# Performance work log

Measured on AMD Instinct MI355X. Metric: run time of the kernel, lower is better.

The kernel has to match this reference:

```python
import math
import jax, jax.numpy as jnp
from jax import lax
import numpy as np

L, B, S, D, H, F = 12, 8, 512, 768, 12, 3072
DH = D // H
REL_POS_BINS, MAX_REL_POS = 32, 128
REL_2D_POS_BINS, MAX_REL_2D_POS = 64, 256
LN_EPS = 1e-12


def _rel_bucket(rel, num_buckets, max_distance):
    # bidirectional relative_position_bucket as in LayoutLMv2
    num_buckets = num_buckets // 2
    ret = (rel > 0).astype(jnp.int32) * num_buckets
    n = jnp.abs(rel)
    max_exact = num_buckets // 2
    is_small = n < max_exact
    n_safe = jnp.maximum(n, 1)  # avoid log(0); masked by is_small anyway
    val_if_large = max_exact + (
        jnp.log(n_safe.astype(jnp.float32) / max_exact)
        / math.log(max_distance / max_exact) * (num_buckets - max_exact)
    ).astype(jnp.int32)
    val_if_large = jnp.minimum(val_if_large, num_buckets - 1)
    return ret + jnp.where(is_small, n.astype(jnp.int32), val_if_large)


def _layernorm(x, g, b):
    mu = jnp.mean(x, axis=-1, keepdims=True)
    var = jnp.var(x, axis=-1, keepdims=True)
    return (x - mu) * lax.rsqrt(var + LN_EPS) * g + b


def _encoder(hidden_states, attention_mask, position_ids, bbox,
             qkv_w, q_bias, v_bias, attn_out_w, attn_out_b, ln1_g, ln1_b,
             inter_w, inter_b, ffn_out_w, ffn_out_b, ln2_g, ln2_b,
             rel_pos_table, rel_x_table, rel_y_table):
    b, s, d = hidden_states.shape
    h = rel_pos_table.shape[1]
    dh = d // h
    # 1D relative position bias: [B,H,S,S]
    rel = position_ids[:, None, :] - position_ids[:, :, None]  # [B,S,S], rel[b,i,j]=p[j]-p[i]
    rp = _rel_bucket(rel, REL_POS_BINS, MAX_REL_POS)
    bias = jnp.transpose(rel_pos_table[rp], (0, 3, 1, 2))
    # 2D spatial bias from bbox x (coord 0) and y (coord 3)
    cx = bbox[:, :, 0]
    cy = bbox[:, :, 3]
    bx = _rel_bucket(cx[:, None, :] - cx[:, :, None], REL_2D_POS_BINS, MAX_REL_2D_POS)
    by = _rel_bucket(cy[:, None, :] - cy[:, :, None], REL_2D_POS_BINS, MAX_REL_2D_POS)
    bias = bias + jnp.transpose(rel_x_table[bx] + rel_y_table[by], (0, 3, 1, 2))
    mask = attention_mask.astype(bool)  # [B,1,1,S], True = masked
    inv_sqrt_dh = 1.0 / math.sqrt(dh)

    def layer(carry, p):
        (qw, qb, vb, aow, aob, g1, b1, iw, ib, fow, fob, g2, b2) = p
        qkv = carry @ qw                      # [B,S,3D] (fast_qkv, no bias)
        q, k, v = jnp.split(qkv, 3, axis=-1)
        q = (q + qb) * inv_sqrt_dh
        v = v + vb
        q = q.reshape(b, s, h, dh)
        k = k.reshape(b, s, h, dh)
        v = v.reshape(b, s, h, dh)
        scores = jnp.einsum('bihd,bjhd->bhij', q, k) + bias
        scores = jnp.where(mask, -jnp.inf, scores.astype(jnp.float32))
        probs = jax.nn.softmax(scores, axis=-1).astype(carry.dtype)
        ctx = jnp.einsum('bhij,bjhd->bihd', probs, v).reshape(b, s, d)
        attn = _layernorm(ctx @ aow + aob + carry, g1, b1)
        ff = jax.nn.gelu(attn @ iw + ib, approximate=False)
        out = _layernorm(ff @ fow + fob + attn, g2, b2)
        return out, None

    params = (qkv_w, q_bias, v_bias, attn_out_w, attn_out_b, ln1_g, ln1_b,
              inter_w, inter_b, ffn_out_w, ffn_out_b, ln2_g, ln2_b)
    out, _ = lax.scan(layer, hidden_states, params)
    return out


def setup_inputs() -> dict:
    key = jax.random.key(0)
    ks = jax.random.split(key, 12)
    w = 0.02
    inp = {
        'hidden_states': jax.random.normal(ks[0], (B, S, D), jnp.float32),
        'attention_mask': jax.random.randint(ks[1], (B, 1, 1, S), 0, 2).astype(jnp.int32),
        'position_ids': jnp.broadcast_to(jnp.arange(S, dtype=jnp.int64), (B, S)),
        'bbox': jax.random.randint(ks[2], (B, S, 4), 0, 1000).astype(jnp.int64),
        'qkv_w': jax.random.normal(ks[3], (L, D, 3 * D), jnp.float32) * w,
        'q_bias': jnp.zeros((L, D), jnp.float32),
        'v_bias': jnp.zeros((L, D), jnp.float32),
        'attn_out_w': jax.random.normal(ks[4], (L, D, D), jnp.float32) * w,
        'attn_out_b': jnp.zeros((L, D), jnp.float32),
        'ln1_g': jnp.ones((L, D), jnp.float32),
        'ln1_b': jnp.zeros((L, D), jnp.float32),
        'inter_w': jax.random.normal(ks[5], (L, D, F), jnp.float32) * w,
        'inter_b': jnp.zeros((L, F), jnp.float32),
        'ffn_out_w': jax.random.normal(ks[6], (L, F, D), jnp.float32) * w,
        'ffn_out_b': jnp.zeros((L, D), jnp.float32),
        'ln2_g': jnp.ones((L, D), jnp.float32),
        'ln2_b': jnp.zeros((L, D), jnp.float32),
        'rel_pos_table': jax.random.normal(ks[7], (REL_POS_BINS, H), jnp.float32) * w,
        'rel_x_table': jax.random.normal(ks[8], (REL_2D_POS_BINS, H), jnp.float32) * w,
        'rel_y_table': jax.random.normal(ks[9], (REL_2D_POS_BINS, H), jnp.float32) * w,
    }
    return inp


def reference(hidden_states, attention_mask, position_ids, bbox,
              qkv_w, q_bias, v_bias, attn_out_w, attn_out_b, ln1_g, ln1_b,
              inter_w, inter_b, ffn_out_w, ffn_out_b, ln2_g, ln2_b,
              rel_pos_table, rel_x_table, rel_y_table):
    return _encoder(hidden_states, attention_mask, position_ids, bbox,
                    qkv_w, q_bias, v_bias, attn_out_w, attn_out_b, ln1_g, ln1_b,
                    inter_w, inter_b, ffn_out_w, ffn_out_b, ln2_g, ln2_b,
                    rel_pos_table, rel_x_table, rel_y_table)
```

## Files before the change

kernel.cpp:

```cpp
#include <hip/hip_runtime.h>
#include <hip/hip_bf16.h>
#include <cstdint>

#define LCONST 12
#define BCONST 8
#define SCONST 512
#define DCONST 768
#define HCONST 12
#define FCONST 3072
#define DH 64

typedef __bf16 bf16x8 __attribute__((ext_vector_type(8)));
typedef float f32x4 __attribute__((ext_vector_type(4)));

__device__ __forceinline__ int rbucket(int rel, int nb2, int maxex) {
    int ret = (rel > 0) ? nb2 : 0;
    int n = (rel < 0) ? -rel : rel;
    if (n < maxex) return ret + n;
    const float inv_ln16 = 0.36067376022224085f;
    int v = maxex + (int)(logf((float)n / (float)maxex) * inv_ln16 * (float)(nb2 - maxex));
    if (v > nb2 - 1) v = nb2 - 1;
    return ret + v;
}

__global__ __launch_bounds__(256) void build_idx_kernel(
        const int* __restrict__ pos, const int* __restrict__ bbox,
        int* __restrict__ idx) {
    size_t t = (size_t)blockIdx.x * 256 + threadIdx.x;
    int j = (int)(t & 511);
    int i = (int)((t >> 9) & 511);
    int b = (int)(t >> 18);
    int rp = rbucket(pos[b * SCONST + j] - pos[b * SCONST + i], 16, 8);
    int cxi = bbox[((size_t)b * SCONST + i) * 4 + 0];
    int cxj = bbox[((size_t)b * SCONST + j) * 4 + 0];
    int cyi = bbox[((size_t)b * SCONST + i) * 4 + 3];
    int cyj = bbox[((size_t)b * SCONST + j) * 4 + 3];
    int bx = rbucket(cxj - cxi, 32, 16);
    int by = rbucket(cyj - cyi, 32, 16);
    idx[t] = rp | (bx << 5) | (by << 11);
}

__global__ __launch_bounds__(256) void cvt_kernel(const float* __restrict__ in,
                                                  __bf16* __restrict__ out, int n) {
    int t = blockIdx.x * 256 + threadIdx.x;
    if (t < n) out[t] = (__bf16)in[t];
}

__global__ __launch_bounds__(256) void transpose_cvt_kernel(
        const float* __restrict__ in, __bf16* __restrict__ out, int R, int C) {
    __shared__ float tile[32][33];
    int nct = C >> 5;
    int c0 = (blockIdx.x % nct) << 5;
    int r0 = (blockIdx.x / nct) << 5;
    int tx = threadIdx.x & 31, ty = threadIdx.x >> 5;
#pragma unroll
    for (int i = 0; i < 32; i += 8)
        tile[ty + i][tx] = in[(size_t)(r0 + ty + i) * C + c0 + tx];
    __syncthreads();
#pragma unroll
    for (int i = 0; i < 32; i += 8)
        out[(size_t)(c0 + ty + i) * R + r0 + tx] = (__bf16)tile[tx][ty + i];
}

template <int MODE>
__global__ __launch_bounds__(256) void gemm_kernel(
        const __bf16* __restrict__ A, const __bf16* __restrict__ Bt,
        int M, int N, int K,
        const float* __restrict__ cbias, const float* __restrict__ vbias,
        const float* __restrict__ resid, float* __restrict__ outF,
        __bf16* __restrict__ outQ, __bf16* __restrict__ outK,
        __bf16* __restrict__ outV, __bf16* __restrict__ outB) {
    __shared__ __align__(16) __bf16 As[128 * 32];
    __shared__ __align__(16) __bf16 Bs[128 * 32];
    int tid = threadIdx.x;
    int wid = tid >> 6, lane = tid & 63, quad = lane >> 4, l16 = lane & 15;
    int nTM = M >> 7;
    int tileM = (blockIdx.x % nTM) << 7;
    int tileN = (blockIdx.x / nTM) << 7;
    int wm = wid >> 1, wn = wid & 1;

    int srow = lane >> 2;
    int scol = (lane & 3) << 3;
    const __bf16* Ag = A + (size_t)(tileM + wid * 32 + srow) * K + scol;
    const __bf16* Bg = Bt + (size_t)(tileN + wid * 32 + srow) * K + scol;
    __bf16* Asl = As + (wid * 32 + srow) * 32 + scol;
    __bf16* Bsl = Bs + (wid * 32 + srow) * 32 + scol;

    f32x4 acc[4][4] = {};

    for (int k0 = 0; k0 < K; k0 += 32) {
        uint4 a0 = *(const uint4*)(Ag + k0);
        uint4 a1 = *(const uint4*)(Ag + (size_t)16 * K + k0);
        uint4 b0 = *(const uint4*)(Bg + k0);
        uint4 b1 = *(const uint4*)(Bg + (size_t)16 * K + k0);
        *(uint4*)Asl = a0;
        *(uint4*)(Asl + 16 * 32) = a1;
        *(uint4*)Bsl = b0;
        *(uint4*)(Bsl + 16 * 32) = b1;
        __syncthreads();
        bf16x8 af[4], bfr[4];
#pragma unroll
        for (int mt = 0; mt < 4; mt++)
            af[mt] = *(const bf16x8*)&As[(wm * 64 + mt * 16 + l16) * 32 + quad * 8];
#pragma unroll
        for (int nt = 0; nt < 4; nt++)
            bfr[nt] = *(const bf16x8*)&Bs[(wn * 64 + nt * 16 + l16) * 32 + quad * 8];
#pragma unroll
        for (int mt = 0; mt < 4; mt++)
#pragma unroll
            for (int nt = 0; nt < 4; nt++)
                acc[mt][nt] = __builtin_amdgcn_mfma_f32_16x16x32_bf16(
                        af[mt], bfr[nt], acc[mt][nt], 0, 0, 0);
        __syncthreads();
    }

#pragma unroll
    for (int mt = 0; mt < 4; mt++)
#pragma unroll
        for (int nt = 0; nt < 4; nt++)
#pragma unroll
            for (int r = 0; r < 4; r++) {
                int row = tileM + wm * 64 + mt * 16 + quad * 4 + r;
                int col = tileN + wn * 64 + nt * 16 + l16;
                float v = acc[mt][nt][r];
                if (MODE == 0) {
                    int b = row >> 9, s = row & 511;
                    if (col < 768) {
                        int h = col >> 6, dh = col & 63;
                        float q = (v + cbias[col]) * 0.125f;
                        outQ[(((size_t)b * HCONST + h) * SCONST + s) * DH + dh] = (__bf16)q;
                    } else if (col < 1536) {
                        int c2 = col - 768;
                        int h = c2 >> 6, dh = c2 & 63;
                        outK[(((size_t)b * HCONST + h) * SCONST + s) * DH + dh] = (__bf16)v;
                    } else {
                        int c2 = col - 1536;
                        int h = c2 >> 6, dh = c2 & 63;
                        float vv = v + vbias[c2];
                        outV[(((size_t)b * HCONST + h) * DH + dh) * SCONST + s] = (__bf16)vv;
                    }
                } else if (MODE == 1 || MODE == 3) {
                    size_t o = (size_t)row * N + col;
                    outF[o] = v + cbias[col] + resid[o];
                } else {
                    float u = v + cbias[col];
                    float g = 0.5f * u * (1.0f + erff(u * 0.70710678118654752f));
                    outB[(size_t)row * N + col] = (__bf16)g;
                }
            }
}

__global__ __launch_bounds__(256) void attn_kernel(
        const __bf16* __restrict__ qbuf, const __bf16* __restrict__ kbuf,
        const __bf16* __restrict__ vbuf, const int* __restrict__ idx,
        const int* __restrict__ amask, const float* __restrict__ tpg,
        const float* __restrict__ txg, const float* __restrict__ tyg,
        __bf16* __restrict__ ctx) {
    int bh = blockIdx.x >> 3;
    int i0 = (blockIdx.x & 7) << 6;
    int b = bh / HCONST, h = bh % HCONST;

    __shared__ __align__(16) __bf16 Ks[64 * 64];
    __shared__ __align__(16) __bf16 Vs[64 * 64];
    __shared__ __align__(16) __bf16 Ps[4][16 * 64];
    __shared__ float tp[32], tx[64], ty[64];
    __shared__ float mk[512];

    int tid = threadIdx.x;
    if (tid < 32) tp[tid] = tpg[tid * HCONST + h];
    if (tid < 64) {
        tx[tid] = txg[tid * HCONST + h];
        ty[tid] = tyg[tid * HCONST + h];
    }
    for (int j = tid; j < 512; j += 256)
        mk[j] = amask[b * SCONST + j] ? -INFINITY : 0.0f;
    __syncthreads();

    int wid = tid >> 6, lane = tid & 63, quad = lane >> 4, l16 = lane & 15;

    const __bf16* qrow = qbuf + ((size_t)bh * SCONST + i0 + wid * 16 + l16) * DH;
    bf16x8 qf0 = *(const bf16x8*)(qrow + quad * 8);
    bf16x8 qf1 = *(const bf16x8*)(qrow + 32 + quad * 8);

    const __bf16* kg = kbuf + (size_t)bh * SCONST * DH;
    const __bf16* vg = vbuf + (size_t)bh * DH * SCONST;

    f32x4 O[4] = {};
    float m_r[4] = {-1e30f, -1e30f, -1e30f, -1e30f};
    float l_r[4] = {0.f, 0.f, 0.f, 0.f};

    for (int j0 = 0; j0 < SCONST; j0 += 64) {
        const uint4* ksrc = (const uint4*)(kg + (size_t)j0 * DH);
        ((uint4*)Ks)[tid] = ksrc[tid];
        ((uint4*)Ks)[tid + 256] = ksrc[tid + 256];
        for (int c = tid; c < 512; c += 256) {
            int dh = c >> 3, cc = c & 7;
            ((uint4*)Vs)[c] = *(const uint4*)(vg + (size_t)dh * SCONST + j0 + cc * 8);
        }
        __syncthreads();

        float sc[4][4];
#pragma unroll
        for (int jt = 0; jt < 4; jt++) {
            f32x4 a = {};
            bf16x8 kf0 = *(const bf16x8*)&Ks[(jt * 16 + l16) * 64 + quad * 8];
            bf16x8 kf1 = *(const bf16x8*)&Ks[(jt * 16 + l16) * 64 + 32 + quad * 8];
            a = __builtin_amdgcn_mfma_f32_16x16x32_bf16(qf0, kf0, a, 0, 0, 0);
            a = __builtin_amdgcn_mfma_f32_16x16x32_bf16(qf1, kf1, a, 0, 0, 0);
#pragma unroll
            for (int r = 0; r < 4; r++) {
                int i = i0 + wid * 16 + quad * 4 + r;
                int j = j0 + jt * 16 + l16;
                int pk = idx[((size_t)b * SCONST + i) * SCONST + j];
                float bias = tp[pk & 31] + tx[(pk >> 5) & 63] + ty[(pk >> 11) & 63];
                sc[jt][r] = a[r] + bias + mk[j];
            }
        }

        float p[4][4];
#pragma unroll
        for (int r = 0; r < 4; r++) {
            float mb = fmaxf(fmaxf(sc[0][r], sc[1][r]), fmaxf(sc[2][r], sc[3][r]));
#pragma unroll
            for (int m = 1; m < 16; m <<= 1) mb = fmaxf(mb, __shfl_xor(mb, m, 64));
            float mn = fmaxf(m_r[r], mb);
            float alpha = __expf(m_r[r] - mn);
            m_r[r] = mn;
            float ls = 0.f;
#pragma unroll
            for (int jt = 0; jt < 4; jt++) {
                float pv = __expf(sc[jt][r] - mn);
                p[jt][r] = pv;
                ls += pv;
            }
#pragma unroll
            for (int m = 1; m < 16; m <<= 1) ls += __shfl_xor(ls, m, 64);
            l_r[r] = l_r[r] * alpha + ls;
#pragma unroll
            for (int nt = 0; nt < 4; nt++) O[nt][r] *= alpha;
        }

        __bf16* pl = &Ps[wid][0];
#pragma unroll
        for (int jt = 0; jt < 4; jt++)
#pragma unroll
            for (int r = 0; r < 4; r++)
                pl[(quad * 4 + r) * 64 + jt * 16 + l16] = (__bf16)p[jt][r];

        bf16x8 pa0 = *(const bf16x8*)&pl[l16 * 64 + quad * 8];
        bf16x8 pa1 = *(const bf16x8*)&pl[l16 * 64 + 32 + quad * 8];
#pragma unroll
        for (int nt = 0; nt < 4; nt++) {
            bf16x8 vb0 = *(const bf16x8*)&Vs[(nt * 16 + l16) * 64 + quad * 8];
            bf16x8 vb1 = *(const bf16x8*)&Vs[(nt * 16 + l16) * 64 + 32 + quad * 8];
            O[nt] = __builtin_amdgcn_mfma_f32_16x16x32_bf16(pa0, vb0, O[nt], 0, 0, 0);
            O[nt] = __builtin_amdgcn_mfma_f32_16x16x32_bf16(pa1, vb1, O[nt], 0, 0, 0);
        }
        __syncthreads();
    }

#pragma unroll
    for (int nt = 0; nt < 4; nt++)
#pragma unroll
        for (int r = 0; r < 4; r++) {
            int i = i0 + wid * 16 + quad * 4 + r;
            int dh = nt * 16 + l16;
            float o = O[nt][r] / l_r[r];
            ctx[((size_t)b * SCONST + i) * DCONST + h * DH + dh] = (__bf16)o;
        }
}

__global__ __launch_bounds__(256) void ln_kernel(
        const float* __restrict__ in, const float* __restrict__ g,
        const float* __restrict__ bb, float* __restrict__ outF,
        __bf16* __restrict__ outB) {
    __shared__ float red[4];
    int row = blockIdx.x, t = threadIdx.x;
    const float* x = in + (size_t)row * DCONST;
    float v0 = x[t], v1 = x[t + 256], v2 = x[t + 512];
    float s = v0 + v1 + v2;
#pragma unroll
    for (int m = 1; m < 64; m <<= 1) s += __shfl_xor(s, m, 64);
    if ((t & 63) == 0) red[t >> 6] = s;
    __syncthreads();
    s = red[0] + red[1] + red[2] + red[3];
    __syncthreads();
    float mu = s * (1.0f / 768.0f);
    float d0 = v0 - mu, d1 = v1 - mu, d2 = v2 - mu;
    float q = d0 * d0 + d1 * d1 + d2 * d2;
#pragma unroll
    for (int m = 1; m < 64; m <<= 1) q += __shfl_xor(q, m, 64);
    if ((t & 63) == 0) red[t >> 6] = q;
    __syncthreads();
    q = red[0] + red[1] + red[2] + red[3];
    float rstd = rsqrtf(q * (1.0f / 768.0f) + 1e-12f);
    float y0 = d0 * rstd * g[t] + bb[t];
    float y1 = d1 * rstd * g[t + 256] + bb[t + 256];
    float y2 = d2 * rstd * g[t + 512] + bb[t + 512];
    size_t o = (size_t)row * DCONST;
    outF[o + t] = y0;
    outF[o + t + 256] = y1;
    outF[o + t + 512] = y2;
    outB[o + t] = (__bf16)y0;
    outB[o + t + 256] = (__bf16)y1;
    outB[o + t + 512] = (__bf16)y2;
}

extern "C" void kernel_launch(void* const* d_in, const int* in_sizes, int n_in,
                              void* d_out, int out_size, void* d_ws, size_t ws_size,
                              hipStream_t stream) {
    const float* hidden = (const float*)d_in[0];
    const int* amask = (const int*)d_in[1];
    const int* pos = (const int*)d_in[2];
    const int* bbox = (const int*)d_in[3];
    const float* qkv_w = (const float*)d_in[4];
    const float* q_bias = (const float*)d_in[5];
    const float* v_bias = (const float*)d_in[6];
    const float* aow = (const float*)d_in[7];
    const float* aob = (const float*)d_in[8];
    const float* ln1g = (const float*)d_in[9];
    const float* ln1b = (const float*)d_in[10];
    const float* iw = (const float*)d_in[11];
    const float* ib = (const float*)d_in[12];
    const float* fow = (const float*)d_in[13];
    const float* fob = (const float*)d_in[14];
    const float* ln2g = (const float*)d_in[15];
    const float* ln2b = (const float*)d_in[16];
    const float* tpt = (const float*)d_in[17];
    const float* txt = (const float*)d_in[18];
    const float* tyt = (const float*)d_in[19];
    float* out = (float*)d_out;

    char* w = (char*)d_ws;
    auto carve = [&](size_t bytes) {
        char* p = w;
        w += (bytes + 255) & ~(size_t)255;
        return p;
    };
    const size_t MT = 4096;
    __bf16* wqT = (__bf16*)carve((size_t)2304 * 768 * 2);
    __bf16* waT = (__bf16*)carve((size_t)768 * 768 * 2);
    __bf16* wiT = (__bf16*)carve((size_t)3072 * 768 * 2);
    __bf16* wfT = (__bf16*)carve((size_t)768 * 3072 * 2);
    __bf16* qbuf = (__bf16*)carve(MT * 768 * 2);
    __bf16* kbuf = (__bf16*)carve(MT * 768 * 2);
    __bf16* vbuf = (__bf16*)carve(MT * 768 * 2);
    __bf16* xbf = (__bf16*)carve(MT * 768 * 2);
    __bf16* ctxbf = (__bf16*)carve(MT * 768 * 2);
    float* attnf = (float*)carve(MT * 768 * 4);
    __bf16* attnbf = (__bf16*)carve(MT * 768 * 2);
    __bf16* ffbf = (__bf16*)carve(MT * 3072 * 2);
    float* t1 = (float*)carve(MT * 768 * 4);
    int* idxb = (int*)carve((size_t)BCONST * SCONST * SCONST * 4);

    build_idx_kernel<<<(BCONST * SCONST * SCONST) / 256, 256, 0, stream>>>(pos, bbox, idxb);
    cvt_kernel<<<(int)(MT * 768 / 256), 256, 0, stream>>>(hidden, xbf, (int)(MT * 768));

    for (int l = 0; l < LCONST; l++) {
        transpose_cvt_kernel<<<(2304 / 32) * (768 / 32), 256, 0, stream>>>(
                qkv_w + (size_t)l * 768 * 2304, wqT, 768, 2304);
        transpose_cvt_kernel<<<(768 / 32) * (768 / 32), 256, 0, stream>>>(
                aow + (size_t)l * 768 * 768, waT, 768, 768);
        transpose_cvt_kernel<<<(3072 / 32) * (768 / 32), 256, 0, stream>>>(
                iw + (size_t)l * 768 * 3072, wiT, 768, 3072);
        transpose_cvt_kernel<<<(768 / 32) * (3072 / 32), 256, 0, stream>>>(
                fow + (size_t)l * 3072 * 768, wfT, 3072, 768);

        gemm_kernel<0><<<(4096 / 128) * (2304 / 128), 256, 0, stream>>>(
                xbf, wqT, 4096, 2304, 768, q_bias + (size_t)l * 768,
                v_bias + (size_t)l * 768, nullptr, nullptr, qbuf, kbuf, vbuf, nullptr);

        attn_kernel<<<BCONST * HCONST * (SCONST / 64), 256, 0, stream>>>(
                qbuf, kbuf, vbuf, idxb, amask, tpt, txt, tyt, ctxbf);

        const float* xres = (l == 0) ? hidden : out;
        gemm_kernel<1><<<(4096 / 128) * (768 / 128), 256, 0, stream>>>(
                ctxbf, waT, 4096, 768, 768, aob + (size_t)l * 768, nullptr, xres, t1,
                nullptr, nullptr, nullptr, nullptr);
        ln_kernel<<<4096, 256, 0, stream>>>(t1, ln1g + (size_t)l * 768,
                                            ln1b + (size_t)l * 768, attnf, attnbf);

        gemm_kernel<2><<<(4096 / 128) * (3072 / 128), 256, 0, stream>>>(
                attnbf, wiT, 4096, 3072, 768, ib + (size_t)l * 3072, nullptr, nullptr,
                nullptr, nullptr, nullptr, nullptr, ffbf);

        gemm_kernel<3><<<(4096 / 128) * (768 / 128), 256, 0, stream>>>(
                ffbf, wfT, 4096, 768, 3072, fob + (size_t)l * 768, nullptr, attnf, t1,
                nullptr, nullptr, nullptr, nullptr);
        ln_kernel<<<4096, 256, 0, stream>>>(t1, ln2g + (size_t)l * 768,
                                            ln2b + (size_t)l * 768, out, xbf);
    }
}
```

Baseline: 3.249 ms.

## Use direct global-to-LDS loads in GEMM and attention, batch weight conversion

```diff
diff --git a/kernel.cpp b/kernel.cpp
--- a/kernel.cpp
+++ b/kernel.cpp
@@ -12,6 +12,12 @@
 
 typedef __bf16 bf16x8 __attribute__((ext_vector_type(8)));
 typedef float f32x4 __attribute__((ext_vector_type(4)));
+
+__device__ __forceinline__ void gload16(const void* g, void* l) {
+    __builtin_amdgcn_global_load_lds(
+            (const __attribute__((address_space(1))) void*)g,
+            (__attribute__((address_space(3))) void*)l, 16, 0, 0);
+}
 
 __device__ __forceinline__ int rbucket(int rel, int nb2, int maxex) {
     int ret = (rel > 0) ? nb2 : 0;
@@ -49,17 +55,18 @@
 __global__ __launch_bounds__(256) void transpose_cvt_kernel(
         const float* __restrict__ in, __bf16* __restrict__ out, int R, int C) {
     __shared__ float tile[32][33];
+    size_t off = (size_t)blockIdx.y * R * C;
     int nct = C >> 5;
     int c0 = (blockIdx.x % nct) << 5;
     int r0 = (blockIdx.x / nct) << 5;
     int tx = threadIdx.x & 31, ty = threadIdx.x >> 5;
 #pragma unroll
     for (int i = 0; i < 32; i += 8)
-        tile[ty + i][tx] = in[(size_t)(r0 + ty + i) * C + c0 + tx];
+        tile[ty + i][tx] = in[off + (size_t)(r0 + ty + i) * C + c0 + tx];
     __syncthreads();
 #pragma unroll
     for (int i = 0; i < 32; i += 8)
-        out[(size_t)(c0 + ty + i) * R + r0 + tx] = (__bf16)tile[tx][ty + i];
+        out[off + (size_t)(c0 + ty + i) * R + r0 + tx] = (__bf16)tile[tx][ty + i];
 }
 
 template <int MODE>
@@ -79,24 +86,18 @@
     int tileN = (blockIdx.x / nTM) << 7;
     int wm = wid >> 1, wn = wid & 1;
 
-    int srow = lane >> 2;
-    int scol = (lane & 3) << 3;
-    const __bf16* Ag = A + (size_t)(tileM + wid * 32 + srow) * K + scol;
-    const __bf16* Bg = Bt + (size_t)(tileN + wid * 32 + srow) * K + scol;
-    __bf16* Asl = As + (wid * 32 + srow) * 32 + scol;
-    __bf16* Bsl = Bs + (wid * 32 + srow) * 32 + scol;
+    const __bf16* gA0 = A + (size_t)(tileM + wid * 32 + (lane >> 2)) * K + ((lane & 3) << 3);
+    const __bf16* gB0 = Bt + (size_t)(tileN + wid * 32 + (lane >> 2)) * K + ((lane & 3) << 3);
+    __bf16* lA0 = As + wid * 1024;
+    __bf16* lB0 = Bs + wid * 1024;
 
     f32x4 acc[4][4] = {};
 
     for (int k0 = 0; k0 < K; k0 += 32) {
-        uint4 a0 = *(const uint4*)(Ag + k0);
-        uint4 a1 = *(const uint4*)(Ag + (size_t)16 * K + k0);
-        uint4 b0 = *(const uint4*)(Bg + k0);
-        uint4 b1 = *(const uint4*)(Bg + (size_t)16 * K + k0);
-        *(uint4*)Asl = a0;
-        *(uint4*)(Asl + 16 * 32) = a1;
-        *(uint4*)Bsl = b0;
-        *(uint4*)(Bsl + 16 * 32) = b1;
+        gload16(gA0 + k0, lA0);
+        gload16(gA0 + (size_t)16 * K + k0, lA0 + 512);
+        gload16(gB0 + k0, lB0);
+        gload16(gB0 + (size_t)16 * K + k0, lB0 + 512);
         __syncthreads();
         bf16x8 af[4], bfr[4];
 #pragma unroll
@@ -174,7 +175,6 @@
     }
     for (int j = tid; j < 512; j += 256)
         mk[j] = amask[b * SCONST + j] ? -INFINITY : 0.0f;
-    __syncthreads();
 
     int wid = tid >> 6, lane = tid & 63, quad = lane >> 4, l16 = lane & 15;
 
@@ -189,13 +189,18 @@
     float m_r[4] = {-1e30f, -1e30f, -1e30f, -1e30f};
     float l_r[4] = {0.f, 0.f, 0.f, 0.f};
 
+    __syncthreads();
+
     for (int j0 = 0; j0 < SCONST; j0 += 64) {
-        const uint4* ksrc = (const uint4*)(kg + (size_t)j0 * DH);
-        ((uint4*)Ks)[tid] = ksrc[tid];
-        ((uint4*)Ks)[tid + 256] = ksrc[tid + 256];
-        for (int c = tid; c < 512; c += 256) {
-            int dh = c >> 3, cc = c & 7;
-            ((uint4*)Vs)[c] = *(const uint4*)(vg + (size_t)dh * SCONST + j0 + cc * 8);
+        {
+            const __bf16* kbase = kg + (size_t)j0 * DH;
+#pragma unroll
+            for (int s = 0; s < 2; s++) {
+                int c = wid * 2 + s;
+                gload16(kbase + c * 512 + lane * 8, Ks + c * 512);
+                int dh = c * 8 + (lane >> 3), cc = lane & 7;
+                gload16(vg + (size_t)dh * SCONST + j0 + cc * 8, Vs + c * 512);
+            }
         }
         __syncthreads();
 
@@ -332,16 +337,13 @@
     float* out = (float*)d_out;
 
     char* w = (char*)d_ws;
+    size_t used = 0;
     auto carve = [&](size_t bytes) {
-        char* p = w;
-        w += (bytes + 255) & ~(size_t)255;
+        char* p = w + used;
+        used += (bytes + 255) & ~(size_t)255;
         return p;
     };
     const size_t MT = 4096;
-    __bf16* wqT = (__bf16*)carve((size_t)2304 * 768 * 2);
-    __bf16* waT = (__bf16*)carve((size_t)768 * 768 * 2);
-    __bf16* wiT = (__bf16*)carve((size_t)3072 * 768 * 2);
-    __bf16* wfT = (__bf16*)carve((size_t)768 * 3072 * 2);
     __bf16* qbuf = (__bf16*)carve(MT * 768 * 2);
     __bf16* kbuf = (__bf16*)carve(MT * 768 * 2);
     __bf16* vbuf = (__bf16*)carve(MT * 768 * 2);
@@ -353,21 +355,50 @@
     float* t1 = (float*)carve(MT * 768 * 4);
     int* idxb = (int*)carve((size_t)BCONST * SCONST * SCONST * 4);
 
+    const size_t wq_sz = (size_t)2304 * 768 * 2;
+    const size_t wa_sz = (size_t)768 * 768 * 2;
+    const size_t wi_sz = (size_t)3072 * 768 * 2;
+    const size_t wf_sz = (size_t)768 * 3072 * 2;
+    const size_t wsum = wq_sz + wa_sz + wi_sz + wf_sz;
+    bool full = (ws_size >= used + 12 * wsum + (12 * 4 + 4) * 256);
+    int nlw = full ? 12 : 1;
+    __bf16* wqT = (__bf16*)carve(wq_sz * nlw);
+    __bf16* waT = (__bf16*)carve(wa_sz * nlw);
+    __bf16* wiT = (__bf16*)carve(wi_sz * nlw);
+    __bf16* wfT = (__bf16*)carve(wf_sz * nlw);
+
     build_idx_kernel<<<(BCONST * SCONST * SCONST) / 256, 256, 0, stream>>>(pos, bbox, idxb);
     cvt_kernel<<<(int)(MT * 768 / 256), 256, 0, stream>>>(hidden, xbf, (int)(MT * 768));
 
+    if (full) {
+        transpose_cvt_kernel<<<dim3((2304 / 32) * (768 / 32), 12), 256, 0, stream>>>(
+                qkv_w, wqT, 768, 2304);
+        transpose_cvt_kernel<<<dim3((768 / 32) * (768 / 32), 12), 256, 0, stream>>>(
+                aow, waT, 768, 768);
+        transpose_cvt_kernel<<<dim3((3072 / 32) * (768 / 32), 12), 256, 0, stream>>>(
+                iw, wiT, 768, 3072);
+        transpose_cvt_kernel<<<dim3((768 / 32) * (3072 / 32), 12), 256, 0, stream>>>(
+                fow, wfT, 3072, 768);
+    }
+
     for (int l = 0; l < LCONST; l++) {
-        transpose_cvt_kernel<<<(2304 / 32) * (768 / 32), 256, 0, stream>>>(
-                qkv_w + (size_t)l * 768 * 2304, wqT, 768, 2304);
-        transpose_cvt_kernel<<<(768 / 32) * (768 / 32), 256, 0, stream>>>(
-                aow + (size_t)l * 768 * 768, waT, 768, 768);
-        transpose_cvt_kernel<<<(3072 / 32) * (768 / 32), 256, 0, stream>>>(
-                iw + (size_t)l * 768 * 3072, wiT, 768, 3072);
-        transpose_cvt_kernel<<<(768 / 32) * (3072 / 32), 256, 0, stream>>>(
-                fow + (size_t)l * 3072 * 768, wfT, 3072, 768);
+        __bf16* wq_l = wqT + (full ? (size_t)l * 2304 * 768 : 0);
+        __bf16* wa_l = waT + (full ? (size_t)l * 768 * 768 : 0);
+        __bf16* wi_l = wiT + (full ? (size_t)l * 3072 * 768 : 0);
+        __bf16* wf_l = wfT + (full ? (size_t)l * 768 * 3072 : 0);
+        if (!full) {
+            transpose_cvt_kernel<<<dim3((2304 / 32) * (768 / 32), 1), 256, 0, stream>>>(
+                    qkv_w + (size_t)l * 768 * 2304, wq_l, 768, 2304);
+            transpose_cvt_kernel<<<dim3((768 / 32) * (768 / 32), 1), 256, 0, stream>>>(
+                    aow + (size_t)l * 768 * 768, wa_l, 768, 768);
+            transpose_cvt_kernel<<<dim3((3072 / 32) * (768 / 32), 1), 256, 0, stream>>>(
+                    iw + (size_t)l * 768 * 3072, wi_l, 768, 3072);
+            transpose_cvt_kernel<<<dim3((768 / 32) * (3072 / 32), 1), 256, 0, stream>>>(
+                    fow + (size_t)l * 3072 * 768, wf_l, 3072, 768);
+        }
 
         gemm_kernel<0><<<(4096 / 128) * (2304 / 128), 256, 0, stream>>>(
-                xbf, wqT, 4096, 2304, 768, q_bias + (size_t)l * 768,
+                xbf, wq_l, 4096, 2304, 768, q_bias + (size_t)l * 768,
                 v_bias + (size_t)l * 768, nullptr, nullptr, qbuf, kbuf, vbuf, nullptr);
 
         attn_kernel<<<BCONST * HCONST * (SCONST / 64), 256, 0, stream>>>(
@@ -375,17 +406,17 @@
 
         const float* xres = (l == 0) ? hidden : out;
         gemm_kernel<1><<<(4096 / 128) * (768 / 128), 256, 0, stream>>>(
-                ctxbf, waT, 4096, 768, 768, aob + (size_t)l * 768, nullptr, xres, t1,
+                ctxbf, wa_l, 4096, 768, 768, aob + (size_t)l * 768, nullptr, xres, t1,
                 nullptr, nullptr, nullptr, nullptr);
         ln_kernel<<<4096, 256, 0, stream>>>(t1, ln1g + (size_t)l * 768,
                                             ln1b + (size_t)l * 768, attnf, attnbf);
 
         gemm_kernel<2><<<(4096 / 128) * (3072 / 128), 256, 0, stream>>>(
-                attnbf, wiT, 4096, 3072, 768, ib + (size_t)l * 3072, nullptr, nullptr,
+                attnbf, wi_l, 4096, 3072, 768, ib + (size_t)l * 3072, nullptr, nullptr,
                 nullptr, nullptr, nullptr, nullptr, ffbf);
 
         gemm_kernel<3><<<(4096 / 128) * (768 / 128), 256, 0, stream>>>(
-                ffbf, wfT, 4096, 768, 3072, fob + (size_t)l * 768, nullptr, attnf, t1,
+                ffbf, wf_l, 4096, 768, 3072, fob + (size_t)l * 768, nullptr, attnf, t1,
                 nullptr, nullptr, nullptr, nullptr);
         ln_kernel<<<4096, 256, 0, stream>>>(t1, ln2g + (size_t)l * 768,
                                             ln2b + (size_t)l * 768, out, xbf);
```

Result: no change. 3.298 ms (+1.5%).
